# Kernel optimization log

Measured on AMD Instinct MI355X. Metric: run time of the kernel, lower is better.

Reference implementation:

```python
import jax, jax.numpy as jnp
import numpy as np

B, T = 4096, 20
X_DIM, Z_DIM, H_DIM = 256, 128, 512
ZL, HL = 64, 64
D = X_DIM + Z_DIM  # 384, size of A


def _linear_params(key, out_f, in_f):
    kw, kb = jax.random.split(key)
    bound = 1.0 / np.sqrt(in_f)
    W = jax.random.uniform(kw, (out_f, in_f), minval=-bound, maxval=bound, dtype=jnp.float32)
    b = jax.random.uniform(kb, (out_f,), minval=-bound, maxval=bound, dtype=jnp.float32)
    return W, b


def setup_inputs() -> dict:
    key = jax.random.key(0)
    ks = jax.random.split(key, 12)
    x = jax.random.normal(ks[0], (B, T, X_DIM), dtype=jnp.float32)
    h_in = jax.random.normal(ks[1], (B, T, HL), dtype=jnp.float32)
    z_in = jax.random.normal(ks[2], (B, T, ZL), dtype=jnp.float32)
    A = jax.random.normal(ks[3], (D, D), dtype=jnp.float32) / np.sqrt(D)
    # Pz_xh_mean_forward: LinearUnit(x+h -> h), LinearUnit(h -> z)
    Wm1, bm1 = _linear_params(ks[4], H_DIM, X_DIM + H_DIM)
    Wm2, bm2 = _linear_params(ks[5], Z_DIM, H_DIM)
    # Pz_xh_logvar_forward: same shapes
    Wv1, bv1 = _linear_params(ks[6], H_DIM, X_DIM + H_DIM)
    Wv2, bv2 = _linear_params(ks[7], Z_DIM, H_DIM)
    # phi_xz_forward: LinearUnit(x+z -> 2h)
    Wphi, bphi = _linear_params(ks[8], 2 * H_DIM, X_DIM + Z_DIM)
    # LSTMCell(2h -> h), torch layout: gates order i, f, g, o
    W_ih, b_ih = _linear_params(ks[9], 4 * H_DIM, 2 * H_DIM)
    W_hh, b_hh = _linear_params(ks[10], 4 * H_DIM, H_DIM)
    return dict(x=x, h_in=h_in, z_in=z_in, A=A,
                Wm1=Wm1, bm1=bm1, Wm2=Wm2, bm2=bm2,
                Wv1=Wv1, bv1=bv1, Wv2=Wv2, bv2=bv2,
                Wphi=Wphi, bphi=bphi,
                W_ih=W_ih, W_hh=W_hh, b_ih=b_ih, b_hh=b_hh)


def _forward(x, h_in, z_in, A, Wm1, bm1, Wm2, bm2, Wv1, bv1, Wv2, bv2,
             Wphi, bphi, W_ih, W_hh, b_ih, b_hh):
    lrelu = lambda v: jax.nn.leaky_relu(v, 0.2)

    def step(carry, x_t):
        h, c = carry  # [B, H] each
        xh = jnp.concatenate([x_t, h], axis=1)                       # [B, X+H]
        mean = lrelu(lrelu(xh @ Wm1.T + bm1) @ Wm2.T + bm2)          # [B, Z]
        logvar = lrelu(lrelu(xh @ Wv1.T + bv1) @ Wv2.T + bv2)        # [B, Z]
        z = mean  # eval mode: reparameterize_gaussian returns the mean
        xz = jnp.concatenate([x_t, z], axis=1)                       # [B, D]
        agg = xz @ A.T  # == matmul(A, xz.T).T                       # [B, D]
        phi = jax.nn.softplus(lrelu(agg @ Wphi.T + bphi))            # [B, 2H]
        gates = phi @ W_ih.T + b_ih + h @ W_hh.T + b_hh              # [B, 4H]
        i, f, g, o = jnp.split(gates, 4, axis=1)
        c_new = jax.nn.sigmoid(f) * c + jax.nn.sigmoid(i) * jnp.tanh(g)
        h_new = jax.nn.sigmoid(o) * jnp.tanh(c_new)
        # h_out records h BEFORE the update (as in the torch loop)
        return (h_new, c_new), (z, mean, logvar, h, h_new)

    h0 = jnp.zeros((x.shape[0], H_DIM), dtype=x.dtype)
    c0 = jnp.zeros((x.shape[0], H_DIM), dtype=x.dtype)
    xT = jnp.swapaxes(x, 0, 1)  # [T, B, X]
    _, (z, mean, logvar, h_out, h_lo) = jax.lax.scan(step, (h0, c0), xT)
    to_bt = lambda a: jnp.swapaxes(a, 0, 1)  # [B, T, *]
    return (to_bt(z), to_bt(mean), to_bt(logvar), to_bt(h_out), to_bt(h_lo))


def reference(x, h_in, z_in, A, Wm1, bm1, Wm2, bm2, Wv1, bv1, Wv2, bv2,
              Wphi, bphi, W_ih, W_hh, b_ih, b_hh):
    return _forward(x, h_in, z_in, A, Wm1, bm1, Wm2, bm2, Wv1, bv1, Wv2, bv2,
                    Wphi, bphi, W_ih, W_hh, b_ih, b_hh)
```

## Files before the change

### kernel.cpp

```cpp
#include <hip/hip_runtime.h>
#include <math.h>

constexpr int B_ = 4096;
constexpr int T_ = 20;
constexpr int XD = 256;
constexpr int ZD = 128;
constexpr int HD = 512;
constexpr int DD = 384;

using short8 = __attribute__((ext_vector_type(8))) short;
using bf16x8 = __attribute__((ext_vector_type(8))) __bf16;
using f32x4  = __attribute__((ext_vector_type(4))) float;

__device__ __forceinline__ float lrelu_f(float v) { return v > 0.f ? v : 0.2f * v; }
__device__ __forceinline__ float softplus_f(float v) {
    return log1pf(expf(-fabsf(v))) + fmaxf(v, 0.f);
}
__device__ __forceinline__ float sigmoid_f(float v) { return 1.f / (1.f + expf(-v)); }

__device__ __forceinline__ unsigned short f2b(float f) {
    unsigned u = __builtin_bit_cast(unsigned, f);
    u += 0x7fff + ((u >> 16) & 1);
    return (unsigned short)(u >> 16);
}

__device__ __forceinline__ f32x4 mfma16(short8 a, short8 b, f32x4 c) {
    return __builtin_amdgcn_mfma_f32_16x16x32_bf16(
        __builtin_bit_cast(bf16x8, a), __builtin_bit_cast(bf16x8, b), c, 0, 0, 0);
}

__device__ __forceinline__ void load_lds16(const unsigned short* g, unsigned short* l) {
    __builtin_amdgcn_global_load_lds(
        (const __attribute__((address_space(1))) unsigned int*)g,
        (__attribute__((address_space(3))) unsigned int*)l,
        16, 0, 0);
}

template <int LPT>
__device__ __forceinline__ void vmwait(int rem) {
    if (rem >= 2) {
        if constexpr (LPT == 4)      asm volatile("s_waitcnt vmcnt(8)" ::: "memory");
        else if constexpr (LPT == 3) asm volatile("s_waitcnt vmcnt(6)" ::: "memory");
        else                         asm volatile("s_waitcnt vmcnt(4)" ::: "memory");
    } else if (rem == 1) {
        if constexpr (LPT == 4)      asm volatile("s_waitcnt vmcnt(4)" ::: "memory");
        else if constexpr (LPT == 3) asm volatile("s_waitcnt vmcnt(3)" ::: "memory");
        else                         asm volatile("s_waitcnt vmcnt(2)" ::: "memory");
    } else {
        asm volatile("s_waitcnt vmcnt(0)" ::: "memory");
    }
}

template <int MT>
__device__ __forceinline__ void gemm_core(
    const unsigned short* A1, int lda1, int K1,
    const unsigned short* A2, int lda2, int K2,
    const unsigned short* W1, int ldw1,
    const unsigned short* W2, int ldw2,
    int bm, int bn,
    unsigned short* As, unsigned short* Bs,
    f32x4 (&acc)[MT / 32][4])
{
    constexpr int MI   = MT / 32;
    constexpr int WRS  = MT / 2;
    constexpr int NA   = MT / 64;
    constexpr int LPT  = NA + 2;
    constexpr int ABUF = MT * 32;

    const int tid  = threadIdx.x;
    const int lane = tid & 63;
    const int wave = tid >> 6;
    const int wr = wave >> 1, wc = wave & 1;
    const int fr = lane & 15, fg = lane >> 4;
    const int cswz = fg ^ ((fr >> 1) & 3);

    const int r0 = tid >> 2,          c0 = (tid & 3) ^ ((r0 >> 1) & 3);
    const int r1 = (256 + tid) >> 2,  c1 = ((256 + tid) & 3) ^ ((r1 >> 1) & 3);

    const int n1 = K1 / 32;
    const int nt = n1 + K2 / 32;

    auto stage = [&](int i, int buf) {
        const unsigned short* Ag;
        const unsigned short* Wg;
        int lda, ldw, kb;
        if (i < n1) { Ag = A1; Wg = W1; lda = lda1; ldw = ldw1; kb = i * 32; }
        else        { Ag = A2; Wg = W2; lda = lda2; ldw = ldw2; kb = (i - n1) * 32; }
        unsigned short* lA = As + buf * ABUF + wave * 512;
        unsigned short* lB = Bs + buf * 4096 + wave * 512;
        load_lds16(Ag + (size_t)(bm + r0) * lda + kb + c0 * 8, lA);
        if constexpr (NA == 2)
            load_lds16(Ag + (size_t)(bm + r1) * lda + kb + c1 * 8, lA + 2048);
        load_lds16(Wg + (size_t)(bn + r0) * ldw + kb + c0 * 8, lB);
        load_lds16(Wg + (size_t)(bn + r1) * ldw + kb + c1 * 8, lB + 2048);
    };

    auto compute = [&](int buf) {
        const unsigned short* Ab_ = As + buf * ABUF;
        const unsigned short* Bb_ = Bs + buf * 4096;
        short8 af[MI], bv[4];
#pragma unroll
        for (int mi = 0; mi < MI; ++mi)
            af[mi] = *reinterpret_cast<const short8*>(Ab_ + (wr * WRS + mi * 16 + fr) * 32 + cswz * 8);
#pragma unroll
        for (int ni = 0; ni < 4; ++ni)
            bv[ni] = *reinterpret_cast<const short8*>(Bb_ + (wc * 64 + ni * 16 + fr) * 32 + cswz * 8);
#pragma unroll
        for (int mi = 0; mi < MI; ++mi)
#pragma unroll
            for (int ni = 0; ni < 4; ++ni)
                acc[mi][ni] = mfma16(af[mi], bv[ni], acc[mi][ni]);
    };

    stage(0, 0);
    if (1 < nt) stage(1, 1);
    if (2 < nt) stage(2, 2);
    {
        int rem = (nt - 1 < 2) ? (nt - 1) : 2;
        vmwait<LPT>(rem);
    }
    __builtin_amdgcn_s_barrier();

    int buf = 0;
    for (int i = 0; i < nt; ++i) {
        compute(buf);
        if (i + 1 < nt) {
            asm volatile("" ::: "memory");
            __builtin_amdgcn_s_barrier();
            if (i + 3 < nt) stage(i + 3, buf);
            int rem = nt - (i + 2);
            if (rem > 2) rem = 2;
            vmwait<LPT>(rem);
            __builtin_amdgcn_s_barrier();
            buf = (buf == 2) ? 0 : buf + 1;
        }
    }
}

__device__ __forceinline__ void gemm_core8w(
    const unsigned short* A1, int lda1, int K1,
    const unsigned short* A2, int lda2, int K2,
    const unsigned short* W1, int ldw1,
    const unsigned short* W2, int ldw2,
    int bm, int bn,
    unsigned short* As, unsigned short* Bs,
    f32x4 (&acc)[2][4])
{
    const int tid  = threadIdx.x;
    const int lane = tid & 63;
    const int wave = tid >> 6;
    const int wr = wave >> 1, wc = wave & 1;
    const int fr = lane & 15, fg = lane >> 4;
    const int cswz = fg ^ ((fr >> 1) & 3);

    const int r0 = tid >> 2;
    const int c0 = (tid & 3) ^ ((r0 >> 1) & 3);

    const int n1 = K1 / 32;
    const int nt = n1 + K2 / 32;

    auto stage = [&](int i, int buf) {
        const unsigned short* Ag;
        const unsigned short* Wg;
        int lda, ldw, kb;
        if (i < n1) { Ag = A1; Wg = W1; lda = lda1; ldw = ldw1; kb = i * 32; }
        else        { Ag = A2; Wg = W2; lda = lda2; ldw = ldw2; kb = (i - n1) * 32; }
        unsigned short* lA = As + buf * 4096 + wave * 512;
        unsigned short* lB = Bs + buf * 4096 + wave * 512;
        load_lds16(Ag + (size_t)(bm + r0) * lda + kb + c0 * 8, lA);
        load_lds16(Wg + (size_t)(bn + r0) * ldw + kb + c0 * 8, lB);
    };

    auto compute = [&](int buf) {
        const unsigned short* Ab_ = As + buf * 4096;
        const unsigned short* Bb_ = Bs + buf * 4096;
        short8 af[2], bv[4];
#pragma unroll
        for (int mi = 0; mi < 2; ++mi)
            af[mi] = *reinterpret_cast<const short8*>(Ab_ + (wr * 32 + mi * 16 + fr) * 32 + cswz * 8);
#pragma unroll
        for (int ni = 0; ni < 4; ++ni)
            bv[ni] = *reinterpret_cast<const short8*>(Bb_ + (wc * 64 + ni * 16 + fr) * 32 + cswz * 8);
#pragma unroll
        for (int mi = 0; mi < 2; ++mi)
#pragma unroll
            for (int ni = 0; ni < 4; ++ni)
                acc[mi][ni] = mfma16(af[mi], bv[ni], acc[mi][ni]);
    };

    stage(0, 0);
    if (1 < nt) stage(1, 1);
    if (2 < nt) stage(2, 2);
    {
        int rem = (nt - 1 < 2) ? (nt - 1) : 2;
        vmwait<2>(rem);
    }
    __builtin_amdgcn_s_barrier();

    int buf = 0;
    for (int i = 0; i < nt; ++i) {
        compute(buf);
        if (i + 1 < nt) {
            asm volatile("" ::: "memory");
            __builtin_amdgcn_s_barrier();
            if (i + 3 < nt) stage(i + 3, buf);
            int rem = nt - (i + 2);
            if (rem > 2) rem = 2;
            vmwait<2>(rem);
            __builtin_amdgcn_s_barrier();
            buf = (buf == 2) ? 0 : buf + 1;
        }
    }
}

template <int ACT, int MT, int NMASK, int NSHIFT>
__global__ __launch_bounds__(256) void k_gemm_act(
    const unsigned short* __restrict__ A1, int lda1, int K1,
    const unsigned short* __restrict__ A2, int lda2, int K2,
    const unsigned short* __restrict__ W1, int ldw1,
    const unsigned short* __restrict__ W2, int ldw2,
    const float* __restrict__ bias,
    unsigned short* __restrict__ DB, int lddb)
{
    __shared__ unsigned short As[3 * MT * 32];
    __shared__ unsigned short Bs[3 * 4096];
    const int id = blockIdx.x;
    const int bm = (id >> NSHIFT) * MT, bn = (id & NMASK) * 128;
    f32x4 acc[MT / 32][4] = {};
    gemm_core<MT>(A1, lda1, K1, A2, lda2, K2, W1, ldw1, W2, ldw2, bm, bn, As, Bs, acc);

    constexpr int MI = MT / 32, WRS = MT / 2;
    const int tid = threadIdx.x, lane = tid & 63, wave = tid >> 6;
    const int wr = wave >> 1, wc = wave & 1, fr = lane & 15, rg = lane >> 4;
    float bb[4];
#pragma unroll
    for (int ni = 0; ni < 4; ++ni)
        bb[ni] = bias ? bias[bn + wc * 64 + ni * 16 + fr] : 0.f;
#pragma unroll
    for (int mi = 0; mi < MI; ++mi)
#pragma unroll
        for (int r = 0; r < 4; ++r) {
            const int row = bm + wr * WRS + mi * 16 + rg * 4 + r;
#pragma unroll
            for (int ni = 0; ni < 4; ++ni) {
                float v = acc[mi][ni][r] + bb[ni];
                if (ACT == 1) v = lrelu_f(v);
                else if (ACT == 2) v = softplus_f(lrelu_f(v));
                DB[(size_t)row * lddb + (bn + wc * 64 + ni * 16 + fr)] = f2b(v);
            }
        }
}

__global__ __launch_bounds__(256) void k_meanphi(
    const unsigned short* __restrict__ uslot,
    const unsigned short* __restrict__ xb,
    const unsigned short* __restrict__ Wm2b,
    const unsigned short* __restrict__ Wcb,
    const float* __restrict__ bm2,
    const float* __restrict__ bphi,
    float* __restrict__ oz, float* __restrict__ om,
    unsigned short* __restrict__ phib)
{
    __shared__ unsigned short As[3 * 64 * 32];
    __shared__ unsigned short Bs[3 * 4096];
    __shared__ unsigned short meanL[64 * 136];

    const int id = blockIdx.x;
    const int bm = (id >> 3) * 64, bn = (id & 7) * 128;
    const int tid = threadIdx.x, lane = tid & 63, wave = tid >> 6;
    const int wr = wave >> 1, wc = wave & 1, fr = lane & 15, fg = lane >> 4, rg = lane >> 4;
    const int cswz = fg ^ ((fr >> 1) & 3);
    const int r0 = tid >> 2,          c0 = (tid & 3) ^ ((r0 >> 1) & 3);
    const int r1 = (256 + tid) >> 2,  c1 = ((256 + tid) & 3) ^ ((r1 >> 1) & 3);

    {
        f32x4 macc[2][4] = {};
        gemm_core<64>(uslot, 1024, 512, uslot, 1024, 0,
                      Wm2b, 512, Wm2b, 512, bm, 0, As, Bs, macc);
        float mb[4];
#pragma unroll
        for (int ni = 0; ni < 4; ++ni)
            mb[ni] = bm2[wc * 64 + ni * 16 + fr];
#pragma unroll
        for (int mi = 0; mi < 2; ++mi)
#pragma unroll
            for (int r = 0; r < 4; ++r) {
                const int rowl = wr * 32 + mi * 16 + rg * 4 + r;
#pragma unroll
                for (int ni = 0; ni < 4; ++ni) {
                    const int col = wc * 64 + ni * 16 + fr;
                    const float v = lrelu_f(macc[mi][ni][r] + mb[ni]);
                    meanL[rowl * 136 + col] = f2b(v);
                    if (bn == 0) {
                        const size_t o = (size_t)(bm + rowl) * (T_ * ZD) + col;
                        oz[o] = v; om[o] = v;
                    }
                }
            }
    }
    __syncthreads();

    f32x4 acc[2][4] = {};
    gemm_core<64>(xb, XD, XD, xb, XD, 0,
                  Wcb, DD, Wcb, DD, bm, bn, As, Bs, acc);
    __syncthreads();

    {
        const unsigned short* WG = Wcb + XD;
        auto stageB = [&](int i, int buf) {
            unsigned short* lB = Bs + buf * 4096 + wave * 512;
            load_lds16(WG + (size_t)(bn + r0) * DD + i * 32 + c0 * 8, lB);
            load_lds16(WG + (size_t)(bn + r1) * DD + i * 32 + c1 * 8, lB + 2048);
        };
        stageB(0, 0); stageB(1, 1); stageB(2, 2);
        vmwait<2>(2);
        __builtin_amdgcn_s_barrier();
        int buf = 0;
        for (int i = 0; i < 4; ++i) {
            short8 af[2], bv[4];
#pragma unroll
            for (int mi = 0; mi < 2; ++mi)
                af[mi] = *reinterpret_cast<const short8*>(
                    meanL + (wr * 32 + mi * 16 + fr) * 136 + i * 32 + fg * 8);
#pragma unroll
            for (int ni = 0; ni < 4; ++ni)
                bv[ni] = *reinterpret_cast<const short8*>(
                    Bs + buf * 4096 + (wc * 64 + ni * 16 + fr) * 32 + cswz * 8);
#pragma unroll
            for (int mi = 0; mi < 2; ++mi)
#pragma unroll
                for (int ni = 0; ni < 4; ++ni)
                    acc[mi][ni] = mfma16(af[mi], bv[ni], acc[mi][ni]);
            if (i + 1 < 4) {
                asm volatile("" ::: "memory");
                __builtin_amdgcn_s_barrier();
                if (i + 3 < 4) stageB(i + 3, buf);
                int rem = 4 - (i + 2);
                if (rem > 2) rem = 2;
                vmwait<2>(rem);
                __builtin_amdgcn_s_barrier();
                buf = (buf == 2) ? 0 : buf + 1;
            }
        }
    }

    float pb[4];
#pragma unroll
    for (int ni = 0; ni < 4; ++ni)
        pb[ni] = bphi[bn + wc * 64 + ni * 16 + fr];
#pragma unroll
    for (int mi = 0; mi < 2; ++mi)
#pragma unroll
        for (int r = 0; r < 4; ++r) {
            const int row = bm + wr * 32 + mi * 16 + rg * 4 + r;
#pragma unroll
            for (int ni = 0; ni < 4; ++ni) {
                const float v = softplus_f(lrelu_f(acc[mi][ni][r] + pb[ni]));
                phib[(size_t)row * 1024 + (bn + wc * 64 + ni * 16 + fr)] = f2b(v);
            }
        }
}

__global__ __launch_bounds__(256) void k_logvar_all(
    const unsigned short* __restrict__ umuvall,
    const unsigned short* __restrict__ Wv2b,
    const float* __restrict__ bv2,
    float* __restrict__ out_lv)
{
    __shared__ unsigned short As[3 * 64 * 32];
    __shared__ unsigned short Bs[3 * 4096];
    const int bm = blockIdx.x * 64;
    f32x4 acc[2][4] = {};
    gemm_core<64>(umuvall + 512, 1024, 512, umuvall + 512, 1024, 0,
                  Wv2b, 512, Wv2b, 512, bm, 0, As, Bs, acc);

    const int tid = threadIdx.x, lane = tid & 63, wave = tid >> 6;
    const int wr = wave >> 1, wc = wave & 1, fr = lane & 15, rg = lane >> 4;
    float bb[4];
#pragma unroll
    for (int ni = 0; ni < 4; ++ni)
        bb[ni] = bv2[wc * 64 + ni * 16 + fr];
#pragma unroll
    for (int mi = 0; mi < 2; ++mi)
#pragma unroll
        for (int r = 0; r < 4; ++r) {
            const int row = bm + wr * 32 + mi * 16 + rg * 4 + r;
            const int t = row >> 12, b = row & (B_ - 1);
#pragma unroll
            for (int ni = 0; ni < 4; ++ni) {
                const int col = wc * 64 + ni * 16 + fr;
                out_lv[(size_t)b * (T_ * ZD) + (size_t)t * ZD + col] =
                    lrelu_f(acc[mi][ni][r] + bb[ni]);
            }
        }
}

__global__ __launch_bounds__(512) void k_gates_lstm(
    const unsigned short* __restrict__ phib,
    const unsigned short* __restrict__ hbin,
    const unsigned short* __restrict__ Wih,
    const unsigned short* __restrict__ Whh,
    const float* __restrict__ br,
    float* __restrict__ c,
    unsigned short* __restrict__ hbout,
    float* __restrict__ ohl,
    float* __restrict__ oh_next)
{
    __shared__ unsigned short As[3 * 4096];
    __shared__ unsigned short Bs[3 * 4096];
    const int id = blockIdx.x;
    const int sid = (id & 7) * 64 + (id >> 3);
    const int bm = (sid >> 4) * 128, bn = (sid & 15) * 128;
    f32x4 acc[2][4] = {};
    gemm_core8w(phib, 1024, 1024, hbin, 512, 512, Wih, 1024, Whh, 512, bm, bn, As, Bs, acc);

    const int tid = threadIdx.x, lane = tid & 63, wave = tid >> 6;
    const int wr = wave >> 1, wc = wave & 1, fr = lane & 15, rg = lane >> 4;
    const int n = ((bn + wc * 64) >> 6) * 16 + fr;
    float bb[4];
#pragma unroll
    for (int ni = 0; ni < 4; ++ni)
        bb[ni] = br[bn + wc * 64 + ni * 16 + fr];
#pragma unroll
    for (int mi = 0; mi < 2; ++mi)
#pragma unroll
        for (int r = 0; r < 4; ++r) {
            const int row = bm + wr * 32 + mi * 16 + rg * 4 + r;
            const size_t idx = (size_t)row * HD + n;
            const float gi = acc[mi][0][r] + bb[0];
            const float gf = acc[mi][1][r] + bb[1];
            const float gg = acc[mi][2][r] + bb[2];
            const float go = acc[mi][3][r] + bb[3];
            const float co = c[idx];
            const float cn = sigmoid_f(gf) * co + sigmoid_f(gi) * tanhf(gg);
            const float hn = sigmoid_f(go) * tanhf(cn);
            c[idx] = cn;
            hbout[idx] = f2b(hn);
            const size_t ob = (size_t)row * (T_ * HD) + n;
            ohl[ob] = hn;
            if (oh_next) oh_next[ob] = hn;
        }
}

__global__ __launch_bounds__(256) void k_gemm_plain(
    const unsigned short* __restrict__ A1, int lda1, int K1,
    const unsigned short* __restrict__ W1, int ldw1,
    unsigned short* __restrict__ DB, int lddb)
{
    __shared__ unsigned short As[3 * 128 * 32];
    __shared__ unsigned short Bs[3 * 4096];
    const int bm = blockIdx.y * 128, bn = blockIdx.x * 128;
    f32x4 acc[4][4] = {};
    gemm_core<128>(A1, lda1, K1, A1, lda1, 0, W1, ldw1, W1, ldw1, bm, bn, As, Bs, acc);

    const int tid = threadIdx.x, lane = tid & 63, wave = tid >> 6;
    const int wr = wave >> 1, wc = wave & 1, fr = lane & 15, rg = lane >> 4;
#pragma unroll
    for (int mi = 0; mi < 4; ++mi)
#pragma unroll
        for (int r = 0; r < 4; ++r) {
            const int row = bm + wr * 64 + mi * 16 + rg * 4 + r;
#pragma unroll
            for (int ni = 0; ni < 4; ++ni) {
                const int col = bn + wc * 64 + ni * 16 + fr;
                DB[(size_t)row * lddb + col] = f2b(acc[mi][ni][r]);
            }
        }
}

constexpr int SG0 = 8192;
constexpr int SG1 = SG0 + 20480;
constexpr int SG2 = SG1 + 3072;
constexpr int SG3 = SG2 + 64;
constexpr int SG4 = SG3 + 64;
constexpr int SG5 = SG4 + 384;
constexpr int SG6 = SG5 + 12288;
constexpr int SG7 = SG6 + 576;
constexpr int SG8 = SG7 + 16;

__global__ __launch_bounds__(256) void prep_all(
    const float* __restrict__ x,
    const float* __restrict__ A,
    const float* __restrict__ Wm1, const float* __restrict__ bm1,
    const float* __restrict__ Wm2,
    const float* __restrict__ Wv1, const float* __restrict__ bv1,
    const float* __restrict__ Wv2,
    const float* __restrict__ Wphi,
    const float* __restrict__ Wih, const float* __restrict__ Whh,
    const float* __restrict__ bih, const float* __restrict__ bhh,
    float* __restrict__ c, unsigned short* __restrict__ hb0,
    float* __restrict__ oh0,
    unsigned short* __restrict__ xball,
    unsigned short* __restrict__ Wub,
    unsigned short* __restrict__ Wm2b, unsigned short* __restrict__ Wv2b,
    unsigned short* __restrict__ Wphib,
    unsigned short* __restrict__ Wrih, unsigned short* __restrict__ Wrhh,
    unsigned short* __restrict__ Atb,
    float* __restrict__ bu, float* __restrict__ br)
{
    const int blk = blockIdx.x;
    const int tid = threadIdx.x;

    if (blk < SG0) {
        const int i = blk * 256 + tid;
        c[i] = 0.f; hb0[i] = 0;
        const int b = i >> 9, nn = i & 511;
        oh0[(size_t)b * (T_ * HD) + nn] = 0.f;
    } else if (blk < SG1) {
        const int i = (blk - SG0) * 256 + tid;
        const int d = i & 63;
        const int bt = i >> 6;
        const int b = bt / T_, t = bt % T_;
        float4 v = reinterpret_cast<const float4*>(x)[i];
        ushort4 o;
        o.x = f2b(v.x); o.y = f2b(v.y); o.z = f2b(v.z); o.w = f2b(v.w);
        reinterpret_cast<ushort4*>(xball)[((size_t)t * B_ + b) * (XD / 4) + d] = o;
    } else if (blk < SG2) {
        const int e = (blk - SG1) * 256 + tid;
        const float v = e < 512 * 768 ? Wm1[e] : Wv1[e - 512 * 768];
        Wub[e] = f2b(v);
    } else if (blk < SG3) {
        const int i = (blk - SG2) * 256 + tid;
        float4 v = reinterpret_cast<const float4*>(Wm2)[i];
        ushort4 o;
        o.x = f2b(v.x); o.y = f2b(v.y); o.z = f2b(v.z); o.w = f2b(v.w);
        reinterpret_cast<ushort4*>(Wm2b)[i] = o;
    } else if (blk < SG4) {
        const int i = (blk - SG3) * 256 + tid;
        float4 v = reinterpret_cast<const float4*>(Wv2)[i];
        ushort4 o;
        o.x = f2b(v.x); o.y = f2b(v.y); o.z = f2b(v.z); o.w = f2b(v.w);
        reinterpret_cast<ushort4*>(Wv2b)[i] = o;
    } else if (blk < SG5) {
        const int i = (blk - SG4) * 256 + tid;
        float4 v = reinterpret_cast<const float4*>(Wphi)[i];
        ushort4 o;
        o.x = f2b(v.x); o.y = f2b(v.y); o.z = f2b(v.z); o.w = f2b(v.w);
        reinterpret_cast<ushort4*>(Wphib)[i] = o;
    } else if (blk < SG6) {
        const int e = (blk - SG5) * 256 + tid;
        const int cc = e / 1536, kk = e % 1536;
        const int gate = (cc >> 4) & 3;
        const int n = ((cc >> 6) << 4) + (cc & 15);
        const int orig = gate * 512 + n;
        if (kk < 1024) Wrih[(size_t)cc * 1024 + kk] = f2b(Wih[(size_t)orig * 1024 + kk]);
        else           Wrhh[(size_t)cc * 512 + (kk - 1024)] = f2b(Whh[(size_t)orig * 512 + (kk - 1024)]);
    } else if (blk < SG7) {
        const int i = (blk - SG6) * 256 + tid;
        const int k = i / DD, j = i % DD;
        Atb[(size_t)k * DD + j] = f2b(A[(size_t)j * DD + k]);
    } else {
        const int i = (blk - SG7) * 256 + tid;
        if (i < 1024) {
            bu[i] = i < 512 ? bm1[i] : bv1[i - 512];
        } else if (i >= 2048) {
            const int cb = i - 2048;
            const int gate = (cb >> 4) & 3;
            const int n = ((cb >> 6) << 4) + (cb & 15);
            const int orig = gate * 512 + n;
            br[cb] = bih[orig] + bhh[orig];
        }
    }
}

extern "C" void kernel_launch(void* const* d_in, const int* in_sizes, int n_in,
                              void* d_out, int out_size, void* d_ws, size_t ws_size,
                              hipStream_t stream)
{
    const float* x    = (const float*)d_in[0];
    const float* A    = (const float*)d_in[3];
    const float* Wm1  = (const float*)d_in[4];
    const float* bm1  = (const float*)d_in[5];
    const float* Wm2  = (const float*)d_in[6];
    const float* bm2  = (const float*)d_in[7];
    const float* Wv1  = (const float*)d_in[8];
    const float* bv1  = (const float*)d_in[9];
    const float* Wv2  = (const float*)d_in[10];
    const float* bv2  = (const float*)d_in[11];
    const float* Wphi = (const float*)d_in[12];
    const float* bphi = (const float*)d_in[13];
    const float* W_ih = (const float*)d_in[14];
    const float* W_hh = (const float*)d_in[15];
    const float* b_ih = (const float*)d_in[16];
    const float* b_hh = (const float*)d_in[17];

    float* out = (float*)d_out;
    float* out_z    = out;
    float* out_mean = out_z + (size_t)B_ * T_ * ZD;
    float* out_lv   = out_mean + (size_t)B_ * T_ * ZD;
    float* out_hout = out_lv + (size_t)B_ * T_ * ZD;
    float* out_hlo  = out_hout + (size_t)B_ * T_ * HD;

    char* wp = (char*)d_ws;
    auto alloc_f = [&](size_t n) { float* p = (float*)wp; wp += n * sizeof(float); return p; };
    auto alloc_b = [&](size_t n) { unsigned short* p = (unsigned short*)wp; wp += n * sizeof(unsigned short); return p; };

    float* c = alloc_f((size_t)B_ * HD);
    unsigned short* hb0     = alloc_b((size_t)B_ * HD);
    unsigned short* hb1     = alloc_b((size_t)B_ * HD);
    unsigned short* xball   = alloc_b((size_t)T_ * B_ * XD);
    unsigned short* umuvall = alloc_b((size_t)T_ * B_ * 1024);
    unsigned short* phib    = alloc_b((size_t)B_ * 1024);

    unsigned short* Wub   = alloc_b((size_t)1024 * 768);
    unsigned short* Wm2b  = alloc_b((size_t)ZD * HD);
    unsigned short* Wv2b  = alloc_b((size_t)ZD * HD);
    unsigned short* Atb   = alloc_b((size_t)DD * DD);
    unsigned short* Wphib = alloc_b((size_t)1024 * DD);
    unsigned short* Wcb   = alloc_b((size_t)1024 * DD);
    unsigned short* Wrih  = alloc_b((size_t)2048 * 1024);
    unsigned short* Wrhh  = alloc_b((size_t)2048 * 512);

    float* bu = alloc_f(1024);
    float* br = alloc_f(2048);

    const dim3 blk(256);

    prep_all<<<dim3(SG8), blk, 0, stream>>>(
        x, A, Wm1, bm1, Wm2, Wv1, bv1, Wv2, Wphi, W_ih, W_hh, b_ih, b_hh,
        c, hb0, out_hout, xball, Wub, Wm2b, Wv2b, Wphib, Wrih, Wrhh, Atb, bu, br);
    k_gemm_plain<<<dim3(DD / 128, 1024 / 128), blk, 0, stream>>>(
        Wphib, DD, DD, Atb, DD, Wcb, DD);

    for (int t = 0; t < T_; ++t) {
        unsigned short* hbt = (t & 1) ? hb1 : hb0;
        unsigned short* hbn = (t & 1) ? hb0 : hb1;
        const unsigned short* xb = xball + (size_t)t * B_ * XD;
        unsigned short* uslot = umuvall + (size_t)t * B_ * 1024;

        k_gemm_act<1, 64, 7, 3><<<dim3(512), blk, 0, stream>>>(
            xb, XD, XD, hbt, HD, HD,
            Wub, XD + HD, Wub + XD, XD + HD,
            bu, uslot, 1024);

        k_meanphi<<<dim3(512), blk, 0, stream>>>(
            uslot, xb, Wm2b, Wcb, bm2, bphi,
            out_z + (size_t)t * ZD, out_mean + (size_t)t * ZD, phib);

        k_gates_lstm<<<dim3(512), dim3(512), 0, stream>>>(
            phib, hbt, Wrih, Wrhh, br,
            c, hbn,
            out_hlo + (size_t)t * HD,
            (t + 1 < T_) ? out_hout + (size_t)(t + 1) * HD : nullptr);
    }

    k_logvar_all<<<dim3(T_ * B_ / 64), blk, 0, stream>>>(
        umuvall, Wv2b, bv2, out_lv);
}
```

Measured before the change: 1.888 ms.

## Use 8-wave blocks with producer/consumer split for the per-step U GEMM

Replaces the 4-wave 64x128 GEMM for the first hidden projection with a 512-thread variant. Each wave computes a 16x64 sub-tile, and the loads are split so waves 0-3 stage the A tile and waves 4-7 stage the W tile through global_load_lds. This doubles the waves per block and shortens each wave's MFMA chain, aiming for better latency hiding. The cost is lower MFMA work per wave, more barrier participants and duplicated B-fragment LDS reads across waves.

Measured after the change: 1.887 ms. Within noise of the previous version (-0.1%).

```diff
diff --git a/kernel.cpp b/kernel.cpp
--- a/kernel.cpp
+++ b/kernel.cpp
@@ -41,11 +41,13 @@
     if (rem >= 2) {
         if constexpr (LPT == 4)      asm volatile("s_waitcnt vmcnt(8)" ::: "memory");
         else if constexpr (LPT == 3) asm volatile("s_waitcnt vmcnt(6)" ::: "memory");
-        else                         asm volatile("s_waitcnt vmcnt(4)" ::: "memory");
+        else if constexpr (LPT == 2) asm volatile("s_waitcnt vmcnt(4)" ::: "memory");
+        else                         asm volatile("s_waitcnt vmcnt(2)" ::: "memory");
     } else if (rem == 1) {
         if constexpr (LPT == 4)      asm volatile("s_waitcnt vmcnt(4)" ::: "memory");
         else if constexpr (LPT == 3) asm volatile("s_waitcnt vmcnt(3)" ::: "memory");
-        else                         asm volatile("s_waitcnt vmcnt(2)" ::: "memory");
+        else if constexpr (LPT == 2) asm volatile("s_waitcnt vmcnt(2)" ::: "memory");
+        else                         asm volatile("s_waitcnt vmcnt(1)" ::: "memory");
     } else {
         asm volatile("s_waitcnt vmcnt(0)" ::: "memory");
     }
@@ -213,6 +215,91 @@
     }
 }
 
+__device__ __forceinline__ void gemm_core8w64(
+    const unsigned short* A1, int lda1, int K1,
+    const unsigned short* A2, int lda2, int K2,
+    const unsigned short* W1, int ldw1,
+    const unsigned short* W2, int ldw2,
+    int bm, int bn,
+    unsigned short* As, unsigned short* Bs,
+    f32x4 (&acc)[1][4])
+{
+    const int tid  = threadIdx.x;
+    const int lane = tid & 63;
+    const int wave = tid >> 6;
+    const int wr = wave >> 1, wc = wave & 1;
+    const int fr = lane & 15, fg = lane >> 4;
+    const int cswz = fg ^ ((fr >> 1) & 3);
+
+    const int ca = wave * 64 + lane;
+    const int ar = ca >> 2, ac = (ca & 3) ^ ((ar >> 1) & 3);
+    const int g0 = (wave - 4) * 2, g1 = g0 + 1;
+    const int cb0 = g0 * 64 + lane, cb1 = g1 * 64 + lane;
+    const int br0 = cb0 >> 2, bc0 = (cb0 & 3) ^ ((br0 >> 1) & 3);
+    const int br1 = cb1 >> 2, bc1 = (cb1 & 3) ^ ((br1 >> 1) & 3);
+
+    const int n1 = K1 / 32;
+    const int nt = n1 + K2 / 32;
+
+    auto stage = [&](int i, int buf) {
+        const unsigned short* Ag;
+        const unsigned short* Wg;
+        int lda, ldw, kb;
+        if (i < n1) { Ag = A1; Wg = W1; lda = lda1; ldw = ldw1; kb = i * 32; }
+        else        { Ag = A2; Wg = W2; lda = lda2; ldw = ldw2; kb = (i - n1) * 32; }
+        if (wave < 4) {
+            unsigned short* lA = As + buf * 2048 + wave * 512;
+            load_lds16(Ag + (size_t)(bm + ar) * lda + kb + ac * 8, lA);
+        } else {
+            unsigned short* lB = Bs + buf * 4096;
+            load_lds16(Wg + (size_t)(bn + br0) * ldw + kb + bc0 * 8, lB + g0 * 512);
+            load_lds16(Wg + (size_t)(bn + br1) * ldw + kb + bc1 * 8, lB + g1 * 512);
+        }
+    };
+
+    auto wait = [&](int rem) {
+        if (wave < 4) vmwait<1>(rem);
+        else          vmwait<2>(rem);
+    };
+
+    auto compute = [&](int buf) {
+        const unsigned short* Ab_ = As + buf * 2048;
+        const unsigned short* Bb_ = Bs + buf * 4096;
+        short8 af = *reinterpret_cast<const short8*>(Ab_ + (wr * 16 + fr) * 32 + cswz * 8);
+        short8 bv[4];
+#pragma unroll
+        for (int ni = 0; ni < 4; ++ni)
+            bv[ni] = *reinterpret_cast<const short8*>(Bb_ + (wc * 64 + ni * 16 + fr) * 32 + cswz * 8);
+#pragma unroll
+        for (int ni = 0; ni < 4; ++ni)
+            acc[0][ni] = mfma16(af, bv[ni], acc[0][ni]);
+    };
+
+    stage(0, 0);
+    if (1 < nt) stage(1, 1);
+    if (2 < nt) stage(2, 2);
+    {
+        int rem = (nt - 1 < 2) ? (nt - 1) : 2;
+        wait(rem);
+    }
+    __builtin_amdgcn_s_barrier();
+
+    int buf = 0;
+    for (int i = 0; i < nt; ++i) {
+        compute(buf);
+        if (i + 1 < nt) {
+            asm volatile("" ::: "memory");
+            __builtin_amdgcn_s_barrier();
+            if (i + 3 < nt) stage(i + 3, buf);
+            int rem = nt - (i + 2);
+            if (rem > 2) rem = 2;
+            wait(rem);
+            __builtin_amdgcn_s_barrier();
+            buf = (buf == 2) ? 0 : buf + 1;
+        }
+    }
+}
+
 template <int ACT, int MT, int NMASK, int NSHIFT>
 __global__ __launch_bounds__(256) void k_gemm_act(
     const unsigned short* __restrict__ A1, int lda1, int K1,
@@ -249,6 +336,38 @@
                 DB[(size_t)row * lddb + (bn + wc * 64 + ni * 16 + fr)] = f2b(v);
             }
         }
+}
+
+__global__ __launch_bounds__(512) void k_u_8w(
+    const unsigned short* __restrict__ A1, int lda1, int K1,
+    const unsigned short* __restrict__ A2, int lda2, int K2,
+    const unsigned short* __restrict__ W1, int ldw1,
+    const unsigned short* __restrict__ W2, int ldw2,
+    const float* __restrict__ bias,
+    unsigned short* __restrict__ DB, int lddb)
+{
+    __shared__ unsigned short As[3 * 2048];
+    __shared__ unsigned short Bs[3 * 4096];
+    const int id = blockIdx.x;
+    const int bm = (id >> 3) * 64, bn = (id & 7) * 128;
+    f32x4 acc[1][4] = {};
+    gemm_core8w64(A1, lda1, K1, A2, lda2, K2, W1, ldw1, W2, ldw2, bm, bn, As, Bs, acc);
+
+    const int tid = threadIdx.x, lane = tid & 63, wave = tid >> 6;
+    const int wr = wave >> 1, wc = wave & 1, fr = lane & 15, rg = lane >> 4;
+    float bb[4];
+#pragma unroll
+    for (int ni = 0; ni < 4; ++ni)
+        bb[ni] = bias[bn + wc * 64 + ni * 16 + fr];
+#pragma unroll
+    for (int r = 0; r < 4; ++r) {
+        const int row = bm + wr * 16 + rg * 4 + r;
+#pragma unroll
+        for (int ni = 0; ni < 4; ++ni) {
+            float v = lrelu_f(acc[0][ni][r] + bb[ni]);
+            DB[(size_t)row * lddb + (bn + wc * 64 + ni * 16 + fr)] = f2b(v);
+        }
+    }
 }
 
 __global__ __launch_bounds__(256) void k_meanphi(
@@ -628,7 +747,7 @@
         const unsigned short* xb = xball + (size_t)t * B_ * XD;
         unsigned short* uslot = umuvall + (size_t)t * B_ * 1024;
 
-        k_gemm_act<1, 64, 7, 3><<<dim3(512), blk, 0, stream>>>(
+        k_u_8w<<<dim3(512), dim3(512), 0, stream>>>(
             xb, XD, XD, hbt, HD, HD,
             Wub, XD + HD, Wub + XD, XD + HD,
             bu, uslot, 1024);
```
